# Optimization experiments

Measured on AMD Instinct MI355X. Metric: run time of the kernel, lower is better.

Reference implementation:

```python
import jax, jax.numpy as jnp
import numpy as np

K = 64
RADIUS = 0.05
PDF_STD = 0.5657
INV_SCALE = 0.05
EMD_EPS = 0.005
EMD_ITERS = 50
SQRT_2PI = 2.5066282746


def _pw_sqdist(a, b):
    # a: (B,N,3), b: (B,M,3) -> (B,N,M) squared euclidean distances
    d = (jnp.sum(a * a, -1)[:, :, None]
         + jnp.sum(b * b, -1)[:, None, :]
         - 2.0 * jnp.einsum('bnd,bmd->bnm', a, b))
    return jnp.maximum(d, 0.0)


def _knn_idx_dist(pts, k, offset=1):
    # returns knn_idx (B,N,k) and squared distances (B,N,k), skipping `offset`
    # nearest points (offset=1 drops the self-match), matching get_knn_idx_dist.
    d2 = _pw_sqdist(pts, pts)                      # (B,N,N)
    neg_d, idx = jax.lax.top_k(-d2, k + offset)    # ascending distance order
    knn_idx = idx[..., offset:]
    knn_dist = jnp.maximum(-neg_d[..., offset:], 0.0)
    return knn_idx, knn_dist


def _emd_assignment(inputs, preds, eps, iters):
    # Iterative entropic-OT (log-domain Sinkhorn) stand-in for the CUDA auction
    # EMD kernel: assigns each input point to a pred point. Indices only -> no grads.
    inputs = jax.lax.stop_gradient(inputs)
    preds = jax.lax.stop_gradient(preds)
    C = _pw_sqdist(inputs, preds)                  # (B,N,M)
    B, N, M = C.shape
    logK = -C / eps
    log_mu = -jnp.log(jnp.float32(N))
    log_nu = -jnp.log(jnp.float32(M))

    def step(carry, _):
        lu, lv = carry
        lu = log_mu - jax.scipy.special.logsumexp(logK + lv[:, None, :], axis=2)
        lv = log_nu - jax.scipy.special.logsumexp(logK + lu[:, :, None], axis=1)
        return (lu, lv), None

    lu0 = jnp.zeros((B, N), jnp.float32)
    lv0 = jnp.zeros((B, M), jnp.float32)
    (lu, lv), _ = jax.lax.scan(step, (lu0, lv0), None, length=iters)
    plan_log = logK + lu[:, :, None] + lv[:, None, :]
    return jnp.argmax(plan_log, axis=2)            # (B,N) int32


def _forward(preds, inputs):
    B, N, _ = inputs.shape
    # 1) EMD assignment + permute preds
    assignment = _emd_assignment(inputs, preds, EMD_EPS, EMD_ITERS)     # (B,N)
    permuted_preds = jnp.take_along_axis(preds, assignment[..., None], axis=1)  # (B,N,3)

    # 2) stochastic neighborhood
    knn_idx, knn_dist = _knn_idx_dist(inputs, K, offset=1)              # (B,N,K)
    prob = jnp.exp(-(knn_dist / INV_SCALE ** 2) / (2.0 * PDF_STD ** 2)) / (PDF_STD * SQRT_2PI)
    u = jax.random.uniform(jax.random.key(42), prob.shape, dtype=prob.dtype)
    mask = (u < prob).astype(jnp.float32)                               # bernoulli(prob)
    mask_sum = jnp.sum(mask, axis=-1, keepdims=True)
    mask_farthest = jnp.where(mask_sum == 0, 1.0, 0.0)                  # (B,N,1)
    mask = mask.at[..., K - 1].add(mask_farthest[..., 0])

    # 3) group neighbor coords + masked squared-distance reduction
    nbh_pos = jax.vmap(lambda pts, idx: pts[idx])(inputs, knn_idx)      # (B,N,K,3)
    dist = jnp.sum((permuted_preds[:, :, None, :] - nbh_pos) ** 2, axis=-1)  # (B,N,K)
    num_nbh = jnp.sum(mask, axis=-1)                                    # (B,N), >= 1
    avg_dist = jnp.sum(dist * mask, axis=-1) / num_nbh
    return jnp.sum(avg_dist)


def setup_inputs() -> dict:
    key = jax.random.key(0)
    k1, k2 = jax.random.split(key)
    inputs = jax.random.normal(k1, (4, 2048, 3), dtype=jnp.float32)
    preds = jax.random.normal(k2, (4, 2048, 3), dtype=jnp.float32)
    return {"preds": preds, "inputs": inputs, "epoch": 10}


def reference(preds, inputs, epoch):
    return _forward(preds, inputs)
```

## Files before the change

### kernel.cpp

```cpp
#include <hip/hip_runtime.h>
#include <stdint.h>

#define NB   4
#define NPTS 2048
#define NROWS (NB * NPTS)
#define KNN  64
typedef unsigned long long u64;

#define NEG_SCALE_L2E (-288.53900817779268f)
#define TWO_SCALE_L2E (577.07801635558536f)

#define SWZ(i) ((i) + ((i) >> 5))
#define COLV_N (NPTS + NPTS / 32)


__device__ __forceinline__ float wave_sum(float v) {
#pragma unroll
  for (int o = 32; o >= 1; o >>= 1) v += __shfl_xor(v, o);
  return v;
}
__device__ __forceinline__ float fexp2(float x) {
  float r; asm("v_exp_f32 %0, %1" : "=v"(r) : "v"(x)); return r;
}
__device__ __forceinline__ float flog2(float x) {
  float r; asm("v_log_f32 %0, %1" : "=v"(r) : "v"(x)); return r;
}
__device__ __forceinline__ float sqdist(const float4 a, const float4 c) {
  float dot = a.x * c.x + a.y * c.y + a.z * c.z;
  float d   = a.w + c.w - 2.0f * dot;
  return fmaxf(d, 0.0f);
}
__device__ __forceinline__ uint32_t rotl32(uint32_t x, uint32_t d) {
  return (x << d) | (x >> (32u - d));
}
__device__ __forceinline__ int mbcnt64(u64 m) {
  return __builtin_amdgcn_mbcnt_hi((uint32_t)(m >> 32),
         __builtin_amdgcn_mbcnt_lo((uint32_t)m, 0));
}
__device__ __forceinline__ float2 lse_merge(float2 A, float2 B) {
  float nm = fmaxf(A.x, B.x);
  float s  = fmaf(A.y, fexp2(A.x - nm), B.y * fexp2(B.x - nm));
  return make_float2(nm, s);
}
__device__ __forceinline__ float agent_ld(const float* p) {
  return __hip_atomic_load(p, __ATOMIC_RELAXED, __HIP_MEMORY_SCOPE_AGENT);
}
__device__ __forceinline__ void agent_st(float* p, float v) {
  __hip_atomic_store(p, v, __ATOMIC_RELAXED, __HIP_MEMORY_SCOPE_AGENT);
}

__device__ __forceinline__ void gbar_b(uint32_t* bb, int gi, uint32_t phase) {
  __syncthreads();
  if (threadIdx.x == 0) {
    uint32_t* grp  = bb + gi * 32;
    uint32_t* root = bb + 256;
    uint32_t* rel  = bb + 288;
    uint32_t old = __hip_atomic_fetch_add(grp, 1u, __ATOMIC_RELAXED,
                                          __HIP_MEMORY_SCOPE_AGENT);
    if (old == 8u * phase - 1u) {
      uint32_t r = __hip_atomic_fetch_add(root, 1u, __ATOMIC_RELAXED,
                                          __HIP_MEMORY_SCOPE_AGENT);
      if (r == 8u * phase - 1u)
        __hip_atomic_store(rel, phase, __ATOMIC_RELAXED,
                           __HIP_MEMORY_SCOPE_AGENT);
    }
    while (__hip_atomic_load(rel, __ATOMIC_RELAXED,
                             __HIP_MEMORY_SCOPE_AGENT) < phase)
      __builtin_amdgcn_s_sleep(1);
  }
  asm volatile("" ::: "memory");
  __syncthreads();
}


__global__ __launch_bounds__(256) void init_kernel(
    const float* __restrict__ preds, const float* __restrict__ inputs,
    float4* __restrict__ in4, float4* __restrict__ pr4,
    float* __restrict__ lu, float* __restrict__ lv) {
  int i = blockIdx.x * 256 + threadIdx.x;
  if (i >= NROWS) return;
  float ax = inputs[3 * i], ay = inputs[3 * i + 1], az = inputs[3 * i + 2];
  in4[i] = make_float4(ax, ay, az, ax * ax + ay * ay + az * az);
  float px = preds[3 * i], py = preds[3 * i + 1], pz = preds[3 * i + 2];
  pr4[i] = make_float4(px, py, pz, px * px + py * py + pz * pz);
  lu[i] = 0.0f;
  lv[i] = 0.0f;
}

__global__ __launch_bounds__(1024, 4) void sink_fused(
    const float4* __restrict__ in4, const float4* __restrict__ pr4,
    float* __restrict__ lu, float* __restrict__ lv,
    float4* __restrict__ perm4, uint32_t* __restrict__ barcnt) {
  __shared__ float4 cin[COLV_N];
  __shared__ float4 cpr[COLV_N];
  __shared__ float  potv[NPTS];
  __shared__ float2 part[64][33];
  __shared__ float2 q32m[32][33];
  __shared__ float2 q8m[8][33];

  int tid   = threadIdx.x;
  int blk   = blockIdx.x & 63;
  int batch = blockIdx.x >> 6;
  int base  = batch << 11;
  int rblk  = blk << 5;
  int gi    = blk & 7;
  uint32_t* bb = barcnt + (batch << 9);
  int tr = tid & 15, g = tid >> 4;
  int cb = g * 33;

  for (int i = tid; i < NPTS; i += 1024) {
    float4 c = in4[base + i];
    cin[SWZ(i)] = make_float4(c.x, c.y, c.z, NEG_SCALE_L2E * c.w);
    float4 p = pr4[base + i];
    cpr[SWZ(i)] = make_float4(p.x, p.y, p.z, NEG_SCALE_L2E * p.w);
  }
  __syncthreads();

  uint32_t phase = 0;
  for (int it = 0; it < 100; ++it) {
    const float*  pin  = (it & 1) ? lu : lv;
    float*        pout = (it & 1) ? lv : lu;
    const float4* crow = (it & 1) ? cpr : cin;
    const float4* ccol = (it & 1) ? cin : cpr;

    for (int i = tid; i < NPTS; i += 1024)
      potv[i] = agent_ld(&pin[base + i]);
    __syncthreads();

    int rl = rblk + tr * 2;
    float4 a0 = crow[SWZ(rl)];
    float4 a1 = crow[SWZ(rl + 1)];
    float mx0 = -INFINITY, mx1 = -INFINITY;
#pragma unroll
    for (int c = 0; c < 32; ++c) {
      float4 cv = ccol[cb + c];
      float wp = cv.w + potv[g * 32 + c];
      float d0 = a0.x * cv.x + a0.y * cv.y + a0.z * cv.z;
      float d1 = a1.x * cv.x + a1.y * cv.y + a1.z * cv.z;
      mx0 = fmaxf(mx0, fmaf(d0, TWO_SCALE_L2E, wp));
      mx1 = fmaxf(mx1, fmaf(d1, TWO_SCALE_L2E, wp));
    }
    float s0 = 0.f, s1 = 0.f;
#pragma unroll
    for (int c = 0; c < 32; ++c) {
      float4 cv = ccol[cb + c];
      float wp = cv.w + potv[g * 32 + c];
      float d0 = a0.x * cv.x + a0.y * cv.y + a0.z * cv.z;
      float d1 = a1.x * cv.x + a1.y * cv.y + a1.z * cv.z;
      s0 += fexp2(fmaf(d0, TWO_SCALE_L2E, wp - mx0));
      s1 += fexp2(fmaf(d1, TWO_SCALE_L2E, wp - mx1));
    }
    part[g][tr * 2 + 0] = make_float2(mx0, s0);
    part[g][tr * 2 + 1] = make_float2(mx1, s1);
    __syncthreads();
    {
      int row = tid & 31, q = tid >> 5;
      q32m[q][row] = lse_merge(part[2 * q][row], part[2 * q + 1][row]);
    }
    __syncthreads();
    if (tid < 256) {
      int row = tid & 31, h = tid >> 5;
      q8m[h][row] = lse_merge(lse_merge(q32m[4 * h][row], q32m[4 * h + 1][row]),
                              lse_merge(q32m[4 * h + 2][row], q32m[4 * h + 3][row]));
    }
    __syncthreads();
    if (tid < 32) {
      float2 P = q8m[0][tid];
#pragma unroll
      for (int k = 1; k < 8; ++k) P = lse_merge(P, q8m[k][tid]);
      float aw = crow[SWZ(rblk + tid)].w;
      agent_st(&pout[base + rblk + tid], -11.0f - (flog2(P.y) + P.x + aw));
    }
    gbar_b(bb, gi, ++phase);
  }

  for (int i = tid; i < NPTS; i += 1024)
    potv[i] = agent_ld(&lv[base + i]);
  __syncthreads();
  u64* upart = (u64*)&part[0][0];
  u64* uq32  = (u64*)&q32m[0][0];
  u64* uq8   = (u64*)&q8m[0][0];
  {
    int rl = rblk + tr * 2;
    float4 a0 = cin[SWZ(rl)], a1 = cin[SWZ(rl + 1)];
    u64 b0 = 0, b1 = 0;
#pragma unroll
    for (int c = 0; c < 32; ++c) {
      float4 cv = cpr[cb + c];
      int m = g * 32 + c;
      float wp = cv.w + potv[m];
      float y0 = fmaf(a0.x * cv.x + a0.y * cv.y + a0.z * cv.z, TWO_SCALE_L2E, wp);
      float y1 = fmaf(a1.x * cv.x + a1.y * cv.y + a1.z * cv.z, TWO_SCALE_L2E, wp);
      uint32_t u0 = __float_as_uint(y0); u0 = (u0 & 0x80000000u) ? ~u0 : (u0 | 0x80000000u);
      uint32_t u1 = __float_as_uint(y1); u1 = (u1 & 0x80000000u) ? ~u1 : (u1 | 0x80000000u);
      u64 p0 = ((u64)u0 << 32) | (uint32_t)(2047 - m); b0 = p0 > b0 ? p0 : b0;
      u64 p1 = ((u64)u1 << 32) | (uint32_t)(2047 - m); b1 = p1 > b1 ? p1 : b1;
    }
    upart[g * 33 + tr * 2 + 0] = b0;
    upart[g * 33 + tr * 2 + 1] = b1;
  }
  __syncthreads();
  {
    int row = tid & 31, q = tid >> 5;
    u64 A = upart[(2 * q) * 33 + row], B = upart[(2 * q + 1) * 33 + row];
    uq32[q * 33 + row] = A > B ? A : B;
  }
  __syncthreads();
  if (tid < 256) {
    int row = tid & 31, h = tid >> 5;
    u64 A = uq32[(4 * h) * 33 + row],     B = uq32[(4 * h + 1) * 33 + row];
    u64 C = uq32[(4 * h + 2) * 33 + row], D = uq32[(4 * h + 3) * 33 + row];
    u64 M = A > B ? A : B; u64 N = C > D ? C : D;
    uq8[h * 33 + row] = M > N ? M : N;
  }
  __syncthreads();
  if (tid < 32) {
    u64 X = uq8[tid];
#pragma unroll
    for (int k = 1; k < 8; ++k) { u64 Y = uq8[k * 33 + tid]; X = Y > X ? Y : X; }
    int m = 2047 - (int)(X & 0xFFFFFFFFu);
    perm4[base + rblk + tid] = pr4[base + m];
  }
}

__global__ __launch_bounds__(256) void knn_loss_kernel(
    const float4* __restrict__ in4, const float4* __restrict__ perm4,
    float* __restrict__ partials) {
  __shared__ uint32_t hist[4][256];
  __shared__ u64 cand[4][96];
  __shared__ u64 sel[4][64];
  int tid  = threadIdx.x;
  int wid  = tid >> 6, lane = tid & 63;
  int row  = blockIdx.x * 4 + wid;
  int base = row & ~(NPTS - 1);
  const float4* ip = in4 + base;
  float4 a = in4[row];

  float dv[32];
#pragma unroll
  for (int t = 0; t < 32; ++t) dv[t] = sqdist(a, ip[(t << 6) | lane]);

#pragma unroll
  for (int j = 0; j < 4; ++j) hist[wid][lane * 4 + j] = 0u;
  asm volatile("s_waitcnt lgkmcnt(0)" ::: "memory");
#pragma unroll
  for (int t = 0; t < 32; ++t) {
    int key = (int)fminf(sqrtf(dv[t]) * 32.0f, 255.0f);
    atomicAdd(&hist[wid][key], 1u);
  }
  asm volatile("s_waitcnt lgkmcnt(0)" ::: "memory");

  uint32_t h0 = hist[wid][lane * 4 + 0], h1 = hist[wid][lane * 4 + 1];
  uint32_t h2 = hist[wid][lane * 4 + 2], h3 = hist[wid][lane * 4 + 3];
  uint32_t s4 = h0 + h1 + h2 + h3;
  uint32_t cum = s4;
#pragma unroll
  for (int o = 1; o < 64; o <<= 1) {
    uint32_t n = __shfl_up(cum, o);
    if (lane >= o) cum += n;
  }
  u64 bal = __ballot(cum >= 65u);
  int Bstar = 255;
  uint32_t cnt_sel = 0;
  if (bal != 0) {
    int lstar = __ffsll(bal) - 1;
    uint32_t cpx = __shfl(cum - s4, lstar);
    uint32_t g0 = __shfl(h0, lstar), g1 = __shfl(h1, lstar);
    uint32_t g2 = __shfl(h2, lstar), g3 = __shfl(h3, lstar);
    if      (cpx + g0 >= 65u)           { Bstar = 4 * lstar;     cnt_sel = cpx + g0; }
    else if (cpx + g0 + g1 >= 65u)      { Bstar = 4 * lstar + 1; cnt_sel = cpx + g0 + g1; }
    else if (cpx + g0 + g1 + g2 >= 65u) { Bstar = 4 * lstar + 2; cnt_sel = cpx + g0 + g1 + g2; }
    else                                { Bstar = 4 * lstar + 3; cnt_sel = cpx + g0 + g1 + g2 + g3; }
  }
  bool exact = (bal == 0) || (cnt_sel > 96u);

  uint32_t T = 0u;
  if (exact) {
    uint32_t lo = 0u, hi = 0x7F7FFFFFu;
    while (lo < hi) {
      uint32_t mid = lo + ((hi - lo) >> 1);
      int c = 0;
#pragma unroll
      for (int t = 0; t < 32; ++t) c += __popcll(__ballot(__float_as_uint(dv[t]) <= mid));
      if (c >= 65) hi = mid; else lo = mid + 1;
    }
    T = lo;
  }

  int pos = 0;
#pragma unroll
  for (int t = 0; t < 32; ++t) {
    bool pr;
    if (exact) {
      pr = (__float_as_uint(dv[t]) <= T);
    } else {
      int key = (int)fminf(sqrtf(dv[t]) * 32.0f, 255.0f);
      pr = (key <= Bstar);
    }
    u64 m = __ballot(pr);
    if (pr) {
      int idx = pos + mbcnt64(m);
      if (idx < 96)
        cand[wid][idx] = ((u64)__float_as_uint(dv[t]) << 32) | (uint32_t)((t << 6) | lane);
    }
    pos += __popcll(m);
  }
  int nc = pos < 96 ? pos : 96;

  u64 mine0 = (lane < nc) ? cand[wid][lane] : ~0ull;
  u64 mine1 = (lane + 64 < nc) ? cand[wid][lane + 64] : ~0ull;
  int r0 = 0, r1 = 0;
  for (int j = 0; j < nc; ++j) {
    u64 cj = cand[wid][j];
    r0 += (cj < mine0) ? 1 : 0;
    r1 += (cj < mine1) ? 1 : 0;
  }
  if (lane < nc && r0 >= 1 && r0 <= 64) sel[wid][r0 - 1] = mine0;
  if (lane + 64 < nc && r1 >= 1 && r1 <= 64) sel[wid][r1 - 1] = mine1;
  u64 s = sel[wid][lane];
  float kd = __uint_as_float((uint32_t)(s >> 32));
  int   ki = (int)(s & 0xFFFFFFFFu);

  const float C1 = (float)(0.05 * 0.05);
  const float C2 = (float)(2.0 * (0.5657 * 0.5657));
  const float C3 = (float)(0.5657 * 2.5066282746);
  float t2 = (kd / C1) / C2;
  float pr = expf(-t2) / C3;

  uint32_t gid = ((uint32_t)row << 6) | (uint32_t)lane;
  const uint32_t HALF = 262144u;
  bool lo2 = gid < HALF;
  uint32_t c0 = lo2 ? gid : (gid - HALF);
  uint32_t c1 = lo2 ? (gid + HALF) : gid;
  const uint32_t k0 = 0u, k1 = 42u;
  const uint32_t k2 = 0x1BD11BDAu ^ k0 ^ k1;
  uint32_t x0 = c0 + k0, x1 = c1 + k1;
#define TF_RND(rr) { x0 += x1; x1 = rotl32(x1, rr); x1 ^= x0; }
  TF_RND(13) TF_RND(15) TF_RND(26) TF_RND(6)
  x0 += k1; x1 += k2 + 1u;
  TF_RND(17) TF_RND(29) TF_RND(16) TF_RND(24)
  x0 += k2; x1 += k0 + 2u;
  TF_RND(13) TF_RND(15) TF_RND(26) TF_RND(6)
  x0 += k0; x1 += k1 + 3u;
  TF_RND(17) TF_RND(29) TF_RND(16) TF_RND(24)
  x0 += k1; x1 += k2 + 4u;
  TF_RND(13) TF_RND(15) TF_RND(26) TF_RND(6)
  x0 += k2; x1 += k0 + 5u;
#undef TF_RND
  uint32_t bits = lo2 ? x0 : x1;
  float u = __uint_as_float((bits >> 9) | 0x3F800000u) - 1.0f;

  bool msk = (u < pr);
  u64 bmask = __ballot(msk);
  int cnt = __popcll(bmask);
  if (cnt == 0 && lane == KNN - 1) msk = true;
  float num = (cnt == 0) ? 1.0f : (float)cnt;

  float4 nb = ip[ki];
  float4 pp = perm4[row];
  float dx = pp.x - nb.x, dy = pp.y - nb.y, dz = pp.z - nb.z;
  float dist = dx * dx + dy * dy + dz * dz;
  float contrib = msk ? dist : 0.0f;
  contrib = wave_sum(contrib);
  if (lane == 0) partials[row] = contrib / num;
}

__global__ __launch_bounds__(256) void reduce_kernel(
    const float* __restrict__ partials, float* __restrict__ out) {
  __shared__ float sm[4];
  int tid = threadIdx.x;
  float s = 0.0f;
  for (int i = tid; i < NROWS; i += 256) s += partials[i];
  s = wave_sum(s);
  if ((tid & 63) == 0) sm[tid >> 6] = s;
  __syncthreads();
  if (tid == 0) out[0] = (sm[0] + sm[1]) + (sm[2] + sm[3]);
}


extern "C" void kernel_launch(void* const* d_in, const int* in_sizes, int n_in,
                              void* d_out, int out_size, void* d_ws, size_t ws_size,
                              hipStream_t stream) {
  const float* preds  = (const float*)d_in[0];
  const float* inputs = (const float*)d_in[1];
  float* out = (float*)d_out;

  char* ws = (char*)d_ws;
  float4* in4   = (float4*)(ws);
  float4* pr4   = (float4*)(ws + 131072);
  float*  lu    = (float*)(ws + 262144);
  float*  lv    = (float*)(ws + 294912);
  float4* perm4 = (float4*)(ws + 327680);
  uint32_t* barcnt = (uint32_t*)(ws + 458752);
  float* partials  = (float*)(ws + 466944);

  hipMemsetAsync(barcnt, 0, 8192, stream);

  init_kernel<<<NROWS / 256, 256, 0, stream>>>(preds, inputs, in4, pr4, lu, lv);
  sink_fused<<<256, 1024, 0, stream>>>(in4, pr4, lu, lv, perm4, barcnt);
  knn_loss_kernel<<<NROWS / 4, 256, 0, stream>>>(in4, perm4, partials);
  reduce_kernel<<<1, 256, 0, stream>>>(partials, out);
}
```

Before: 745.7 us.

## Use single-pass online logsumexp with deferred rescale and 4-row register tiles

Replaces the two-pass max-then-sum logsumexp with a single pass. It keeps a running max and rescales the sum only when a value exceeds the current max by a threshold. It also precomputes the column weight plus potential into a shared array and prescales the row coordinates. Each thread now handles 4 rows over 16 columns instead of 2 rows over 32, cutting LDS reads and FMAs per element. The cost is data-dependent branches, more registers, a larger partial-reduction buffer, and some exp2 headroom risk from the deferred rescaling.

```diff
diff --git a/kernel.cpp b/kernel.cpp
--- a/kernel.cpp
+++ b/kernel.cpp
@@ -9,6 +9,7 @@
 
 #define NEG_SCALE_L2E (-288.53900817779268f)
 #define TWO_SCALE_L2E (577.07801635558536f)
+#define DEFER_T 24.0f
 
 #define SWZ(i) ((i) + ((i) >> 5))
 #define COLV_N (NPTS + NPTS / 32)
@@ -93,8 +94,8 @@
     float4* __restrict__ perm4, uint32_t* __restrict__ barcnt) {
   __shared__ float4 cin[COLV_N];
   __shared__ float4 cpr[COLV_N];
-  __shared__ float  potv[NPTS];
-  __shared__ float2 part[64][33];
+  __shared__ float  wcol[COLV_N];
+  __shared__ float2 part[128][33];
   __shared__ float2 q32m[32][33];
   __shared__ float2 q8m[8][33];
 
@@ -105,8 +106,10 @@
   int rblk  = blk << 5;
   int gi    = blk & 7;
   uint32_t* bb = barcnt + (batch << 9);
-  int tr = tid & 15, g = tid >> 4;
-  int cb = g * 33;
+  int tr = tid & 7;
+  int g  = tid >> 3;
+  int i0 = g << 4;
+  int cb = i0 + (i0 >> 5);
 
   for (int i = tid; i < NPTS; i += 1024) {
     float4 c = in4[base + i];
@@ -116,6 +119,7 @@
   }
   __syncthreads();
 
+  int rl = rblk + tr * 4;
   uint32_t phase = 0;
   for (int it = 0; it < 100; ++it) {
     const float*  pin  = (it & 1) ? lu : lv;
@@ -124,38 +128,44 @@
     const float4* ccol = (it & 1) ? cin : cpr;
 
     for (int i = tid; i < NPTS; i += 1024)
-      potv[i] = agent_ld(&pin[base + i]);
+      wcol[SWZ(i)] = ccol[SWZ(i)].w + agent_ld(&pin[base + i]);
     __syncthreads();
 
-    int rl = rblk + tr * 2;
-    float4 a0 = crow[SWZ(rl)];
-    float4 a1 = crow[SWZ(rl + 1)];
-    float mx0 = -INFINITY, mx1 = -INFINITY;
-#pragma unroll
-    for (int c = 0; c < 32; ++c) {
+    float4 A0 = crow[SWZ(rl)],     A1 = crow[SWZ(rl + 1)];
+    float4 A2 = crow[SWZ(rl + 2)], A3 = crow[SWZ(rl + 3)];
+    float a0x = A0.x * TWO_SCALE_L2E, a0y = A0.y * TWO_SCALE_L2E, a0z = A0.z * TWO_SCALE_L2E;
+    float a1x = A1.x * TWO_SCALE_L2E, a1y = A1.y * TWO_SCALE_L2E, a1z = A1.z * TWO_SCALE_L2E;
+    float a2x = A2.x * TWO_SCALE_L2E, a2y = A2.y * TWO_SCALE_L2E, a2z = A2.z * TWO_SCALE_L2E;
+    float a3x = A3.x * TWO_SCALE_L2E, a3y = A3.y * TWO_SCALE_L2E, a3z = A3.z * TWO_SCALE_L2E;
+    float mx0 = -INFINITY, mx1 = -INFINITY, mx2 = -INFINITY, mx3 = -INFINITY;
+    float mt0 = -INFINITY, mt1 = -INFINITY, mt2 = -INFINITY, mt3 = -INFINITY;
+    float s0 = 0.f, s1 = 0.f, s2 = 0.f, s3 = 0.f;
+#pragma unroll
+    for (int c = 0; c < 16; ++c) {
       float4 cv = ccol[cb + c];
-      float wp = cv.w + potv[g * 32 + c];
-      float d0 = a0.x * cv.x + a0.y * cv.y + a0.z * cv.z;
-      float d1 = a1.x * cv.x + a1.y * cv.y + a1.z * cv.z;
-      mx0 = fmaxf(mx0, fmaf(d0, TWO_SCALE_L2E, wp));
-      mx1 = fmaxf(mx1, fmaf(d1, TWO_SCALE_L2E, wp));
-    }
-    float s0 = 0.f, s1 = 0.f;
-#pragma unroll
-    for (int c = 0; c < 32; ++c) {
-      float4 cv = ccol[cb + c];
-      float wp = cv.w + potv[g * 32 + c];
-      float d0 = a0.x * cv.x + a0.y * cv.y + a0.z * cv.z;
-      float d1 = a1.x * cv.x + a1.y * cv.y + a1.z * cv.z;
-      s0 += fexp2(fmaf(d0, TWO_SCALE_L2E, wp - mx0));
-      s1 += fexp2(fmaf(d1, TWO_SCALE_L2E, wp - mx1));
-    }
-    part[g][tr * 2 + 0] = make_float2(mx0, s0);
-    part[g][tr * 2 + 1] = make_float2(mx1, s1);
+      float  wc = wcol[cb + c];
+      float y0 = fmaf(a0x, cv.x, fmaf(a0y, cv.y, fmaf(a0z, cv.z, wc)));
+      float y1 = fmaf(a1x, cv.x, fmaf(a1y, cv.y, fmaf(a1z, cv.z, wc)));
+      float y2 = fmaf(a2x, cv.x, fmaf(a2y, cv.y, fmaf(a2z, cv.z, wc)));
+      float y3 = fmaf(a3x, cv.x, fmaf(a3y, cv.y, fmaf(a3z, cv.z, wc)));
+      if (y0 > mt0) { s0 *= fexp2(mx0 - y0); mx0 = y0; mt0 = y0 + DEFER_T; }
+      s0 += fexp2(y0 - mx0);
+      if (y1 > mt1) { s1 *= fexp2(mx1 - y1); mx1 = y1; mt1 = y1 + DEFER_T; }
+      s1 += fexp2(y1 - mx1);
+      if (y2 > mt2) { s2 *= fexp2(mx2 - y2); mx2 = y2; mt2 = y2 + DEFER_T; }
+      s2 += fexp2(y2 - mx2);
+      if (y3 > mt3) { s3 *= fexp2(mx3 - y3); mx3 = y3; mt3 = y3 + DEFER_T; }
+      s3 += fexp2(y3 - mx3);
+    }
+    part[g][tr * 4 + 0] = make_float2(mx0, s0);
+    part[g][tr * 4 + 1] = make_float2(mx1, s1);
+    part[g][tr * 4 + 2] = make_float2(mx2, s2);
+    part[g][tr * 4 + 3] = make_float2(mx3, s3);
     __syncthreads();
     {
       int row = tid & 31, q = tid >> 5;
-      q32m[q][row] = lse_merge(part[2 * q][row], part[2 * q + 1][row]);
+      q32m[q][row] = lse_merge(lse_merge(part[4 * q][row], part[4 * q + 1][row]),
+                               lse_merge(part[4 * q + 2][row], part[4 * q + 3][row]));
     }
     __syncthreads();
     if (tid < 256) {
@@ -175,35 +185,49 @@
   }
 
   for (int i = tid; i < NPTS; i += 1024)
-    potv[i] = agent_ld(&lv[base + i]);
+    wcol[SWZ(i)] = cpr[SWZ(i)].w + agent_ld(&lv[base + i]);
   __syncthreads();
   u64* upart = (u64*)&part[0][0];
   u64* uq32  = (u64*)&q32m[0][0];
   u64* uq8   = (u64*)&q8m[0][0];
   {
-    int rl = rblk + tr * 2;
-    float4 a0 = cin[SWZ(rl)], a1 = cin[SWZ(rl + 1)];
-    u64 b0 = 0, b1 = 0;
-#pragma unroll
-    for (int c = 0; c < 32; ++c) {
+    float4 A0 = cin[SWZ(rl)],     A1 = cin[SWZ(rl + 1)];
+    float4 A2 = cin[SWZ(rl + 2)], A3 = cin[SWZ(rl + 3)];
+    float a0x = A0.x * TWO_SCALE_L2E, a0y = A0.y * TWO_SCALE_L2E, a0z = A0.z * TWO_SCALE_L2E;
+    float a1x = A1.x * TWO_SCALE_L2E, a1y = A1.y * TWO_SCALE_L2E, a1z = A1.z * TWO_SCALE_L2E;
+    float a2x = A2.x * TWO_SCALE_L2E, a2y = A2.y * TWO_SCALE_L2E, a2z = A2.z * TWO_SCALE_L2E;
+    float a3x = A3.x * TWO_SCALE_L2E, a3y = A3.y * TWO_SCALE_L2E, a3z = A3.z * TWO_SCALE_L2E;
+    u64 b0 = 0, b1 = 0, b2 = 0, b3 = 0;
+#pragma unroll
+    for (int c = 0; c < 16; ++c) {
       float4 cv = cpr[cb + c];
-      int m = g * 32 + c;
-      float wp = cv.w + potv[m];
-      float y0 = fmaf(a0.x * cv.x + a0.y * cv.y + a0.z * cv.z, TWO_SCALE_L2E, wp);
-      float y1 = fmaf(a1.x * cv.x + a1.y * cv.y + a1.z * cv.z, TWO_SCALE_L2E, wp);
+      float  wc = wcol[cb + c];
+      uint32_t mtag = (uint32_t)(2047 - (i0 + c));
+      float y0 = fmaf(a0x, cv.x, fmaf(a0y, cv.y, fmaf(a0z, cv.z, wc)));
+      float y1 = fmaf(a1x, cv.x, fmaf(a1y, cv.y, fmaf(a1z, cv.z, wc)));
+      float y2 = fmaf(a2x, cv.x, fmaf(a2y, cv.y, fmaf(a2z, cv.z, wc)));
+      float y3 = fmaf(a3x, cv.x, fmaf(a3y, cv.y, fmaf(a3z, cv.z, wc)));
       uint32_t u0 = __float_as_uint(y0); u0 = (u0 & 0x80000000u) ? ~u0 : (u0 | 0x80000000u);
       uint32_t u1 = __float_as_uint(y1); u1 = (u1 & 0x80000000u) ? ~u1 : (u1 | 0x80000000u);
-      u64 p0 = ((u64)u0 << 32) | (uint32_t)(2047 - m); b0 = p0 > b0 ? p0 : b0;
-      u64 p1 = ((u64)u1 << 32) | (uint32_t)(2047 - m); b1 = p1 > b1 ? p1 : b1;
-    }
-    upart[g * 33 + tr * 2 + 0] = b0;
-    upart[g * 33 + tr * 2 + 1] = b1;
+      uint32_t u2 = __float_as_uint(y2); u2 = (u2 & 0x80000000u) ? ~u2 : (u2 | 0x80000000u);
+      uint32_t u3 = __float_as_uint(y3); u3 = (u3 & 0x80000000u) ? ~u3 : (u3 | 0x80000000u);
+      u64 p0 = ((u64)u0 << 32) | mtag; b0 = p0 > b0 ? p0 : b0;
+      u64 p1 = ((u64)u1 << 32) | mtag; b1 = p1 > b1 ? p1 : b1;
+      u64 p2 = ((u64)u2 << 32) | mtag; b2 = p2 > b2 ? p2 : b2;
+      u64 p3 = ((u64)u3 << 32) | mtag; b3 = p3 > b3 ? p3 : b3;
+    }
+    upart[g * 33 + tr * 4 + 0] = b0;
+    upart[g * 33 + tr * 4 + 1] = b1;
+    upart[g * 33 + tr * 4 + 2] = b2;
+    upart[g * 33 + tr * 4 + 3] = b3;
   }
   __syncthreads();
   {
     int row = tid & 31, q = tid >> 5;
-    u64 A = upart[(2 * q) * 33 + row], B = upart[(2 * q + 1) * 33 + row];
-    uq32[q * 33 + row] = A > B ? A : B;
+    u64 A = upart[(4 * q) * 33 + row],     B = upart[(4 * q + 1) * 33 + row];
+    u64 C = upart[(4 * q + 2) * 33 + row], D = upart[(4 * q + 3) * 33 + row];
+    u64 M = A > B ? A : B; u64 N = C > D ? C : D;
+    uq32[q * 33 + row] = M > N ? M : N;
   }
   __syncthreads();
   if (tid < 256) {
```

After: 1.014 ms. 36.0% more time.
